# Kernel tuning notes

Hardware: AMD Instinct MI355X
Metric: run time of the kernel (lower is better)

## Reference

```python
import jax, jax.numpy as jnp
import numpy as np

NEG_SLOPE = 0.01  # nn.LeakyReLU default


def preprocess_adj(A):
    # D^-1/2 A D^-1/2, expressed as row/col broadcast scaling (same math as
    # the original diag_embed + two matmuls, without the O(N^3) waste)
    d = jnp.sum(A, axis=-1)
    d_inv_sqrt = d ** -0.5
    d_inv_sqrt = jnp.where(jnp.isinf(d_inv_sqrt), 0.0, d_inv_sqrt)
    return d_inv_sqrt[..., :, None] * A * d_inv_sqrt[..., None, :]


def gcn_layer(X, A_norm, W, b, residual=False):
    H = jax.nn.leaky_relu(jnp.einsum('bnd,df->bnf', X, W) + b, NEG_SLOPE)
    out = jnp.einsum('bnm,bmf->bnf', A_norm, H)
    if residual:
        out = out + X
    return out


def setup_inputs() -> dict:
    key = jax.random.key(0)
    ks = jax.random.split(key, 8)
    B, N, D_IN, D_H, D_OUT = 8, 2048, 128, 128, 128
    scale_in = 1.0 / np.sqrt(D_IN)
    scale_h = 1.0 / np.sqrt(D_H)
    return {
        'X': jax.random.normal(ks[0], (B, N, D_IN), dtype=jnp.float32),
        'adj': jax.random.uniform(ks[1], (B, N, N), dtype=jnp.float32),
        'W1': jax.random.uniform(ks[2], (D_IN, D_H), minval=-scale_in, maxval=scale_in),
        'b1': jax.random.uniform(ks[3], (D_H,), minval=-scale_in, maxval=scale_in),
        'W2': jax.random.uniform(ks[4], (D_H, D_H), minval=-scale_h, maxval=scale_h),
        'b2': jax.random.uniform(ks[5], (D_H,), minval=-scale_h, maxval=scale_h),
        'W3': jax.random.uniform(ks[6], (D_H, D_OUT), minval=-scale_h, maxval=scale_h),
        'b3': jax.random.uniform(ks[7], (D_OUT,), minval=-scale_h, maxval=scale_h),
    }


def reference(X, adj, W1, b1, W2, b2, W3, b3):
    # Original recomputes preprocess_adj in every layer; result is identical,
    # we honor the math (compute once since adj is unchanged across layers).
    A_norm = preprocess_adj(adj)
    X = gcn_layer(X, A_norm, W1, b1, residual=False)   # GCNLayer (norm defaults False)
    X = gcn_layer(X, A_norm, W2, b2, residual=True)    # Residual_GCNLayer
    X = gcn_layer(X, A_norm, W3, b3, residual=False)   # GCNLayer
    return X
```

## Files before the change

### kernel.cpp

```cpp
#include <hip/hip_runtime.h>


typedef short bf16x8 __attribute__((ext_vector_type(8)));
typedef float f32x4 __attribute__((ext_vector_type(4)));

static __device__ __forceinline__ float bf2f(unsigned short h) {
    union { unsigned int u; float f; } v; v.u = ((unsigned int)h) << 16; return v.f;
}
static __device__ __forceinline__ unsigned short f2bf(float x) {
    union { float f; unsigned int u; } v; v.f = x;
    return (unsigned short)((v.u + 0x7FFFu + ((v.u >> 16) & 1u)) >> 16);
}

__global__ __launch_bounds__(256) void k_pre(const float* __restrict__ adj,
                                             const float* __restrict__ W1,
                                             const float* __restrict__ W2,
                                             const float* __restrict__ W3,
                                             const float* __restrict__ b1,
                                             const float* __restrict__ b2,
                                             const float* __restrict__ b3,
                                             float* __restrict__ dinv,
                                             unsigned short* __restrict__ adjb,
                                             unsigned short* __restrict__ WT,
                                             float* __restrict__ biasf) {
    if (blockIdx.x >= 16384) {
        const int e = (blockIdx.x - 16384) * 256 + threadIdx.x;
        if (e < 49152) {
            const int w = e >> 14, r = e & 16383;
            const int f = r & 127, k = r >> 7;
            const float* W = (w == 0) ? W1 : ((w == 1) ? W2 : W3);
            WT[w * 16384 + f * 128 + k] = f2bf(W[r]);
        } else if (e < 49536) {
            const int idx = e - 49152;
            const float* bp = (idx < 128) ? b1 : ((idx < 256) ? b2 : b3);
            biasf[idx] = bp[idx & 127];
        }
        return;
    }
    const int row = blockIdx.x;
    const size_t base = (size_t)row * 2048 + threadIdx.x * 8;
    const float4 a = *(const float4*)(adj + base);
    const float4 b = *(const float4*)(adj + base + 4);
    float s = a.x + a.y + a.z + a.w + b.x + b.y + b.z + b.w;
    union { uint4 u; unsigned short h[8]; } pk;
    pk.h[0] = f2bf(a.x); pk.h[1] = f2bf(a.y); pk.h[2] = f2bf(a.z); pk.h[3] = f2bf(a.w);
    pk.h[4] = f2bf(b.x); pk.h[5] = f2bf(b.y); pk.h[6] = f2bf(b.z); pk.h[7] = f2bf(b.w);
    *(uint4*)(adjb + base) = pk.u;
#pragma unroll
    for (int off = 32; off > 0; off >>= 1) s += __shfl_down(s, off);
    __shared__ float ws[4];
    if ((threadIdx.x & 63) == 0) ws[threadIdx.x >> 6] = s;
    __syncthreads();
    if (threadIdx.x == 0) {
        float t = ws[0] + ws[1] + ws[2] + ws[3];
        dinv[row] = (t > 0.f) ? rsqrtf(t) : 0.f;
    }
}

template <int AEXT>
__global__ __launch_bounds__(256) void k_gxw(const void* __restrict__ Asrc,
                                             const unsigned short* __restrict__ WTb,
                                             const float* __restrict__ biasf,
                                             const float* __restrict__ dinv,
                                             unsigned short* __restrict__ HsT) {
    constexpr int LDK = 136;
    __shared__ unsigned short Bs[128 * LDK];

    const int tid  = threadIdx.x;
    const int wave = tid >> 6;
    const int lane = tid & 63;
    const int n_   = lane & 15;
    const int q    = lane >> 4;
    const int wm   = wave >> 1;
    const int ch   = wave & 1;

    const int r0 = blockIdx.x * 32;

#pragma unroll
    for (int it = 0; it < 8; ++it) {
        int task = tid + it * 256;
        int f  = task >> 4;
        int cj = (task & 15) * 8;
        *(uint4*)(&Bs[f * LDK + cj]) = *(const uint4*)(WTb + f * 128 + cj);
    }
    __syncthreads();

    const int arow = r0 + wm * 16 + n_;
    bf16x8 av[4];
#pragma unroll
    for (int s = 0; s < 4; ++s) {
        if (AEXT) {
            const float* p = (const float*)Asrc + (size_t)arow * 128 + s * 32 + q * 8;
            float4 uu = ((const float4*)p)[0], w = ((const float4*)p)[1];
            union { bf16x8 v; unsigned short h[8]; } r;
            r.h[0] = f2bf(uu.x); r.h[1] = f2bf(uu.y); r.h[2] = f2bf(uu.z); r.h[3] = f2bf(uu.w);
            r.h[4] = f2bf(w.x);  r.h[5] = f2bf(w.y);  r.h[6] = f2bf(w.z);  r.h[7] = f2bf(w.w);
            av[s] = r.v;
        } else {
            av[s] = *(const bf16x8*)((const unsigned short*)Asrc + (size_t)arow * 128 + s * 32 + q * 8);
        }
    }

    f32x4 acc[4];
#pragma unroll
    for (int i = 0; i < 4; ++i) acc[i] = (f32x4){0.f, 0.f, 0.f, 0.f};
#pragma unroll
    for (int s = 0; s < 4; ++s) {
#pragma unroll
        for (int nt = 0; nt < 4; ++nt) {
            bf16x8 bv = *(const bf16x8*)(&Bs[(ch * 64 + nt * 16 + n_) * LDK + s * 32 + q * 8]);
            acc[nt] = __builtin_amdgcn_mfma_f32_16x16x32_bf16(av[s], bv, acc[nt], 0, 0, 0);
        }
    }

    const int rbase = r0 + wm * 16 + q * 4;
    float dsc[4];
#pragma unroll
    for (int r = 0; r < 4; ++r) dsc[r] = dinv[rbase + r];
    const int b  = rbase >> 11;
    const int jb = rbase & 2047;
    unsigned short* Hb = HsT + (size_t)b * (128 * 2048);
#pragma unroll
    for (int nt = 0; nt < 4; ++nt) {
        const int f = ch * 64 + nt * 16 + n_;
        const float bf = biasf[f];
        unsigned short pk[4];
#pragma unroll
        for (int r = 0; r < 4; ++r) {
            float v = acc[nt][r] + bf;
            v = (v > 0.f) ? v : 0.01f * v;
            pk[r] = f2bf(v * dsc[r]);
        }
        uint2 uo;
        uo.x = (unsigned int)pk[0] | ((unsigned int)pk[1] << 16);
        uo.y = (unsigned int)pk[2] | ((unsigned int)pk[3] << 16);
        *(uint2*)(Hb + (size_t)f * 2048 + jb) = uo;
    }
}

template <int MODE, int OUT32>
__global__ __launch_bounds__(256) void k_gah(const unsigned short* __restrict__ adjb,
                                             const unsigned short* __restrict__ HsT,
                                             const float* __restrict__ dinv,
                                             const unsigned short* __restrict__ resid,
                                             void* __restrict__ outp) {
    constexpr int LDK = 72;
    constexpr int ASZ = 32 * LDK;
    constexpr int BSZ = 128 * LDK;
    __shared__ unsigned short Sm[2 * (ASZ + BSZ)];

    const int tid  = threadIdx.x;
    const int wave = tid >> 6;
    const int lane = tid & 63;
    const int n_   = lane & 15;
    const int q    = lane >> 4;

    const int bb = blockIdx.x;
    const int b  = bb & 7;
    const int rt = bb >> 3;
    const int row0 = b * 2048 + rt * 32;

    const unsigned short* Ag = adjb + (size_t)row0 * 2048;
    const unsigned short* Bg = HsT + (size_t)b * (128 * 2048);

    const int srow = tid >> 3;
    const int sc   = (tid & 7) * 8;
    const unsigned short* As = Ag + (size_t)srow * 2048 + sc;
    const unsigned short* Bsc = Bg + (size_t)srow * 2048 + sc;
    const int dA = srow * LDK + sc;
    const int dB = ASZ + srow * LDK + sc;

    uint4 rA, rB0, rB1, rB2, rB3;
    rA  = *(const uint4*)(As);
    rB0 = *(const uint4*)(Bsc);
    rB1 = *(const uint4*)(Bsc + 32 * 2048);
    rB2 = *(const uint4*)(Bsc + 64 * 2048);
    rB3 = *(const uint4*)(Bsc + 96 * 2048);
    *(uint4*)(&Sm[dA]) = rA;
    *(uint4*)(&Sm[dB]) = rB0;
    *(uint4*)(&Sm[dB + 32 * LDK]) = rB1;
    *(uint4*)(&Sm[dB + 64 * LDK]) = rB2;
    *(uint4*)(&Sm[dB + 96 * LDK]) = rB3;
    __syncthreads();

    f32x4 acc[2][2];
#pragma unroll
    for (int i = 0; i < 2; ++i)
#pragma unroll
        for (int j = 0; j < 2; ++j) acc[i][j] = (f32x4){0.f, 0.f, 0.f, 0.f};

    const int aoff = n_ * LDK + q * 8;
    const int boff = ASZ + (wave * 32 + n_) * LDK + q * 8;

#pragma unroll 1
    for (int kc = 0; kc < 32; ++kc) {
        const int cur = kc & 1;
        if (kc < 31) {
            const int kn = (kc + 1) * 64;
            rA  = *(const uint4*)(As + kn);
            rB0 = *(const uint4*)(Bsc + kn);
            rB1 = *(const uint4*)(Bsc + 32 * 2048 + kn);
            rB2 = *(const uint4*)(Bsc + 64 * 2048 + kn);
            rB3 = *(const uint4*)(Bsc + 96 * 2048 + kn);
        }
        const unsigned short* sb = &Sm[cur * (ASZ + BSZ)];
#pragma unroll
        for (int s = 0; s < 2; ++s) {
            bf16x8 a0 = *(const bf16x8*)(&sb[aoff + s * 32]);
            bf16x8 a1 = *(const bf16x8*)(&sb[aoff + 16 * LDK + s * 32]);
            bf16x8 b0 = *(const bf16x8*)(&sb[boff + s * 32]);
            bf16x8 b1 = *(const bf16x8*)(&sb[boff + 16 * LDK + s * 32]);
            acc[0][0] = __builtin_amdgcn_mfma_f32_16x16x32_bf16(a0, b0, acc[0][0], 0, 0, 0);
            acc[1][0] = __builtin_amdgcn_mfma_f32_16x16x32_bf16(a1, b0, acc[1][0], 0, 0, 0);
            acc[0][1] = __builtin_amdgcn_mfma_f32_16x16x32_bf16(a0, b1, acc[0][1], 0, 0, 0);
            acc[1][1] = __builtin_amdgcn_mfma_f32_16x16x32_bf16(a1, b1, acc[1][1], 0, 0, 0);
        }
        if (kc < 31) {
            unsigned short* sw = &Sm[(cur ^ 1) * (ASZ + BSZ)];
            *(uint4*)(&sw[dA]) = rA;
            *(uint4*)(&sw[dB]) = rB0;
            *(uint4*)(&sw[dB + 32 * LDK]) = rB1;
            *(uint4*)(&sw[dB + 64 * LDK]) = rB2;
            *(uint4*)(&sw[dB + 96 * LDK]) = rB3;
        }
        __syncthreads();
    }

    const int rb = row0 + q * 4;
    float dsc[2][4];
#pragma unroll
    for (int mi = 0; mi < 2; ++mi)
#pragma unroll
        for (int r = 0; r < 4; ++r) dsc[mi][r] = dinv[rb + mi * 16 + r];
#pragma unroll
    for (int mi = 0; mi < 2; ++mi) {
#pragma unroll
        for (int nj = 0; nj < 2; ++nj) {
            const int f = wave * 32 + nj * 16 + n_;
#pragma unroll
            for (int r = 0; r < 4; ++r) {
                const size_t gr = (size_t)(rb + mi * 16 + r);
                float v = acc[mi][nj][r] * dsc[mi][r];
                if (MODE == 2) v += bf2f(resid[gr * 128 + f]);
                if (OUT32) ((float*)outp)[gr * 128 + f] = v;
                else ((unsigned short*)outp)[gr * 128 + f] = f2bf(v);
            }
        }
    }
}

extern "C" void kernel_launch(void* const* d_in, const int* in_sizes, int n_in,
                              void* d_out, int out_size, void* d_ws, size_t ws_size,
                              hipStream_t stream) {
    const float* X   = (const float*)d_in[0];
    const float* adj = (const float*)d_in[1];
    const float* W1  = (const float*)d_in[2];
    const float* b1  = (const float*)d_in[3];
    const float* W2  = (const float*)d_in[4];
    const float* b2  = (const float*)d_in[5];
    const float* W3  = (const float*)d_in[6];
    const float* b3  = (const float*)d_in[7];

    char* ws = (char*)d_ws;
    unsigned short* adjb  = (unsigned short*)ws;
    float*          dinv  = (float*)(ws + (64u << 20));
    float*          biasf = (float*)(ws + (64u << 20) + (64u << 10));
    unsigned short* WT    = (unsigned short*)(ws + (64u << 20) + (128u << 10));
    unsigned short* HsT   = (unsigned short*)(ws + (64u << 20) + (256u << 10));
    unsigned short* Xa    = (unsigned short*)(ws + (68u << 20) + (256u << 10));
    unsigned short* X2    = (unsigned short*)(ws + (72u << 20) + (256u << 10));

    k_pre<<<16578, 256, 0, stream>>>(adj, W1, W2, W3, b1, b2, b3, dinv, adjb, WT, biasf);

    k_gxw<1><<<512, 256, 0, stream>>>(X, WT, biasf, dinv, HsT);
    k_gah<1, 0><<<512, 256, 0, stream>>>(adjb, HsT, dinv, nullptr, Xa);
    k_gxw<0><<<512, 256, 0, stream>>>(Xa, WT + 16384, biasf + 128, dinv, HsT);
    k_gah<2, 0><<<512, 256, 0, stream>>>(adjb, HsT, dinv, Xa, X2);
    k_gxw<0><<<512, 256, 0, stream>>>(X2, WT + 32768, biasf + 256, dinv, HsT);
    k_gah<1, 1><<<512, 256, 0, stream>>>(adjb, HsT, dinv, nullptr, (float*)d_out);
}
```

Measured before the change: 289.8 us.

## Load B operand directly from global into registers, shrink LDS to A tiles

The H^T (B) operand is no longer staged through shared memory. Each wave loads its own MFMA fragments straight from global memory into registers, prefetched two k-steps ahead, while only the adjacency A tile stays double-buffered in LDS. The loop is unrolled by two with a deeper prefetch distance. This cuts LDS traffic and shared memory size, which may allow higher occupancy. In exchange, each B element is read from global by every wave that needs it, with less coalesced 16-byte accesses per lane, and register pressure rises.

```diff
diff --git a/kernel.cpp b/kernel.cpp
--- a/kernel.cpp
+++ b/kernel.cpp
@@ -146,8 +146,7 @@
                                              void* __restrict__ outp) {
     constexpr int LDK = 72;
     constexpr int ASZ = 32 * LDK;
-    constexpr int BSZ = 128 * LDK;
-    __shared__ unsigned short Sm[2 * (ASZ + BSZ)];
+    __shared__ unsigned short Sm[2 * ASZ];
 
     const int tid  = threadIdx.x;
     const int wave = tid >> 6;
@@ -166,64 +165,87 @@
     const int srow = tid >> 3;
     const int sc   = (tid & 7) * 8;
     const unsigned short* As = Ag + (size_t)srow * 2048 + sc;
-    const unsigned short* Bsc = Bg + (size_t)srow * 2048 + sc;
     const int dA = srow * LDK + sc;
-    const int dB = ASZ + srow * LDK + sc;
-
-    uint4 rA, rB0, rB1, rB2, rB3;
-    rA  = *(const uint4*)(As);
-    rB0 = *(const uint4*)(Bsc);
-    rB1 = *(const uint4*)(Bsc + 32 * 2048);
-    rB2 = *(const uint4*)(Bsc + 64 * 2048);
-    rB3 = *(const uint4*)(Bsc + 96 * 2048);
-    *(uint4*)(&Sm[dA]) = rA;
-    *(uint4*)(&Sm[dB]) = rB0;
-    *(uint4*)(&Sm[dB + 32 * LDK]) = rB1;
-    *(uint4*)(&Sm[dB + 64 * LDK]) = rB2;
-    *(uint4*)(&Sm[dB + 96 * LDK]) = rB3;
+
+    const unsigned short* Bp0 = Bg + (size_t)(wave * 32 + n_) * 2048 + q * 8;
+    const unsigned short* Bp1 = Bp0 + 16 * 2048;
+
+    f32x4 acc[2][2];
+#pragma unroll
+    for (int i = 0; i < 2; ++i)
+#pragma unroll
+        for (int j = 0; j < 2; ++j) acc[i][j] = (f32x4){0.f, 0.f, 0.f, 0.f};
+
+    {
+        uint4 t0 = *(const uint4*)(As);
+        *(uint4*)(&Sm[dA]) = t0;
+    }
+    uint4 rA0 = *(const uint4*)(As + 64);
+    uint4 rA1 = *(const uint4*)(As + 128);
+    bf16x8 p00 = *(const bf16x8*)(Bp0);
+    bf16x8 p01 = *(const bf16x8*)(Bp0 + 32);
+    bf16x8 p02 = *(const bf16x8*)(Bp1);
+    bf16x8 p03 = *(const bf16x8*)(Bp1 + 32);
+    bf16x8 r00 = *(const bf16x8*)(Bp0 + 64);
+    bf16x8 r01 = *(const bf16x8*)(Bp0 + 96);
+    bf16x8 r02 = *(const bf16x8*)(Bp1 + 64);
+    bf16x8 r03 = *(const bf16x8*)(Bp1 + 96);
     __syncthreads();
 
-    f32x4 acc[2][2];
-#pragma unroll
-    for (int i = 0; i < 2; ++i)
-#pragma unroll
-        for (int j = 0; j < 2; ++j) acc[i][j] = (f32x4){0.f, 0.f, 0.f, 0.f};
-
     const int aoff = n_ * LDK + q * 8;
-    const int boff = ASZ + (wave * 32 + n_) * LDK + q * 8;
 
 #pragma unroll 1
-    for (int kc = 0; kc < 32; ++kc) {
-        const int cur = kc & 1;
-        if (kc < 31) {
-            const int kn = (kc + 1) * 64;
-            rA  = *(const uint4*)(As + kn);
-            rB0 = *(const uint4*)(Bsc + kn);
-            rB1 = *(const uint4*)(Bsc + 32 * 2048 + kn);
-            rB2 = *(const uint4*)(Bsc + 64 * 2048 + kn);
-            rB3 = *(const uint4*)(Bsc + 96 * 2048 + kn);
-        }
-        const unsigned short* sb = &Sm[cur * (ASZ + BSZ)];
-#pragma unroll
-        for (int s = 0; s < 2; ++s) {
-            bf16x8 a0 = *(const bf16x8*)(&sb[aoff + s * 32]);
-            bf16x8 a1 = *(const bf16x8*)(&sb[aoff + 16 * LDK + s * 32]);
-            bf16x8 b0 = *(const bf16x8*)(&sb[boff + s * 32]);
-            bf16x8 b1 = *(const bf16x8*)(&sb[boff + 16 * LDK + s * 32]);
-            acc[0][0] = __builtin_amdgcn_mfma_f32_16x16x32_bf16(a0, b0, acc[0][0], 0, 0, 0);
-            acc[1][0] = __builtin_amdgcn_mfma_f32_16x16x32_bf16(a1, b0, acc[1][0], 0, 0, 0);
-            acc[0][1] = __builtin_amdgcn_mfma_f32_16x16x32_bf16(a0, b1, acc[0][1], 0, 0, 0);
-            acc[1][1] = __builtin_amdgcn_mfma_f32_16x16x32_bf16(a1, b1, acc[1][1], 0, 0, 0);
-        }
-        if (kc < 31) {
-            unsigned short* sw = &Sm[(cur ^ 1) * (ASZ + BSZ)];
-            *(uint4*)(&sw[dA]) = rA;
-            *(uint4*)(&sw[dB]) = rB0;
-            *(uint4*)(&sw[dB + 32 * LDK]) = rB1;
-            *(uint4*)(&sw[dB + 64 * LDK]) = rB2;
-            *(uint4*)(&sw[dB + 96 * LDK]) = rB3;
-        }
-        __syncthreads();
+    for (int kc = 0; kc < 32; kc += 2) {
+        {
+            *(uint4*)(&Sm[ASZ + dA]) = rA0;
+            if (kc < 29) rA0 = *(const uint4*)(As + (kc + 3) * 64);
+            const unsigned short* sb = &Sm[0];
+            bf16x8 a00 = *(const bf16x8*)(&sb[aoff]);
+            bf16x8 a10 = *(const bf16x8*)(&sb[aoff + 16 * LDK]);
+            bf16x8 a01 = *(const bf16x8*)(&sb[aoff + 32]);
+            bf16x8 a11 = *(const bf16x8*)(&sb[aoff + 16 * LDK + 32]);
+            acc[0][0] = __builtin_amdgcn_mfma_f32_16x16x32_bf16(a00, p00, acc[0][0], 0, 0, 0);
+            acc[1][0] = __builtin_amdgcn_mfma_f32_16x16x32_bf16(a10, p00, acc[1][0], 0, 0, 0);
+            acc[0][1] = __builtin_amdgcn_mfma_f32_16x16x32_bf16(a00, p02, acc[0][1], 0, 0, 0);
+            acc[1][1] = __builtin_amdgcn_mfma_f32_16x16x32_bf16(a10, p02, acc[1][1], 0, 0, 0);
+            acc[0][0] = __builtin_amdgcn_mfma_f32_16x16x32_bf16(a01, p01, acc[0][0], 0, 0, 0);
+            acc[1][0] = __builtin_amdgcn_mfma_f32_16x16x32_bf16(a11, p01, acc[1][0], 0, 0, 0);
+            acc[0][1] = __builtin_amdgcn_mfma_f32_16x16x32_bf16(a01, p03, acc[0][1], 0, 0, 0);
+            acc[1][1] = __builtin_amdgcn_mfma_f32_16x16x32_bf16(a11, p03, acc[1][1], 0, 0, 0);
+            if (kc < 30) {
+                p00 = *(const bf16x8*)(Bp0 + (kc + 2) * 64);
+                p01 = *(const bf16x8*)(Bp0 + (kc + 2) * 64 + 32);
+                p02 = *(const bf16x8*)(Bp1 + (kc + 2) * 64);
+                p03 = *(const bf16x8*)(Bp1 + (kc + 2) * 64 + 32);
+            }
+            __syncthreads();
+        }
+        {
+            if (kc < 30) {
+                *(uint4*)(&Sm[dA]) = rA1;
+                if (kc < 28) rA1 = *(const uint4*)(As + (kc + 4) * 64);
+            }
+            const unsigned short* sb = &Sm[ASZ];
+            bf16x8 a00 = *(const bf16x8*)(&sb[aoff]);
+            bf16x8 a10 = *(const bf16x8*)(&sb[aoff + 16 * LDK]);
+            bf16x8 a01 = *(const bf16x8*)(&sb[aoff + 32]);
+            bf16x8 a11 = *(const bf16x8*)(&sb[aoff + 16 * LDK + 32]);
+            acc[0][0] = __builtin_amdgcn_mfma_f32_16x16x32_bf16(a00, r00, acc[0][0], 0, 0, 0);
+            acc[1][0] = __builtin_amdgcn_mfma_f32_16x16x32_bf16(a10, r00, acc[1][0], 0, 0, 0);
+            acc[0][1] = __builtin_amdgcn_mfma_f32_16x16x32_bf16(a00, r02, acc[0][1], 0, 0, 0);
+            acc[1][1] = __builtin_amdgcn_mfma_f32_16x16x32_bf16(a10, r02, acc[1][1], 0, 0, 0);
+            acc[0][0] = __builtin_amdgcn_mfma_f32_16x16x32_bf16(a01, r01, acc[0][0], 0, 0, 0);
+            acc[1][0] = __builtin_amdgcn_mfma_f32_16x16x32_bf16(a11, r01, acc[1][0], 0, 0, 0);
+            acc[0][1] = __builtin_amdgcn_mfma_f32_16x16x32_bf16(a01, r03, acc[0][1], 0, 0, 0);
+            acc[1][1] = __builtin_amdgcn_mfma_f32_16x16x32_bf16(a11, r03, acc[1][1], 0, 0, 0);
+            if (kc < 29) {
+                r00 = *(const bf16x8*)(Bp0 + (kc + 3) * 64);
+                r01 = *(const bf16x8*)(Bp0 + (kc + 3) * 64 + 32);
+                r02 = *(const bf16x8*)(Bp1 + (kc + 3) * 64);
+                r03 = *(const bf16x8*)(Bp1 + (kc + 3) * 64 + 32);
+            }
+            __syncthreads();
+        }
     }
 
     const int rb = row0 + q * 4;
```

Result: slower. 326.8 us (+12.8%).

## Use direct global-to-LDS loads with triple buffering and XOR swizzle in aggregation

Applied to the files above, without the earlier changes.

Replaces register-staged global loads plus LDS stores in the A·H aggregation kernel with global_load_lds DMA into a three-stage LDS ring. The layout switches from padded rows to an XOR-swizzled unpadded layout to avoid bank conflicts. Waits use a manual vmcnt and raw barriers, and launch bounds now request two blocks per CU. This is meant to cut VGPR pressure and instruction overhead and to deepen load overlap. It relies on precise waitcnt accounting, and the wrap-around prefetch at the end of the loop issues redundant loads.

```diff
diff --git a/kernel.cpp b/kernel.cpp
--- a/kernel.cpp
+++ b/kernel.cpp
@@ -10,6 +10,13 @@
 static __device__ __forceinline__ unsigned short f2bf(float x) {
     union { float f; unsigned int u; } v; v.f = x;
     return (unsigned short)((v.u + 0x7FFFu + ((v.u >> 16) & 1u)) >> 16);
+}
+
+static __device__ __forceinline__ void gl2lds16(const unsigned short* g,
+                                                unsigned short* l) {
+    __builtin_amdgcn_global_load_lds(
+        (const __attribute__((address_space(1))) unsigned int*)g,
+        (__attribute__((address_space(3))) unsigned int*)l, 16, 0, 0);
 }
 
 __global__ __launch_bounds__(256) void k_pre(const float* __restrict__ adj,
@@ -139,15 +146,13 @@
 }
 
 template <int MODE, int OUT32>
-__global__ __launch_bounds__(256) void k_gah(const unsigned short* __restrict__ adjb,
-                                             const unsigned short* __restrict__ HsT,
-                                             const float* __restrict__ dinv,
-                                             const unsigned short* __restrict__ resid,
-                                             void* __restrict__ outp) {
-    constexpr int LDK = 72;
-    constexpr int ASZ = 32 * LDK;
-    constexpr int BSZ = 128 * LDK;
-    __shared__ unsigned short Sm[2 * (ASZ + BSZ)];
+__global__ __launch_bounds__(256, 2) void k_gah(const unsigned short* __restrict__ adjb,
+                                                const unsigned short* __restrict__ HsT,
+                                                const float* __restrict__ dinv,
+                                                const unsigned short* __restrict__ resid,
+                                                void* __restrict__ outp) {
+    constexpr int BUFE = 10240;
+    __shared__ unsigned short Sm[3 * BUFE];
 
     const int tid  = threadIdx.x;
     const int wave = tid >> 6;
@@ -163,25 +168,28 @@
     const unsigned short* Ag = adjb + (size_t)row0 * 2048;
     const unsigned short* Bg = HsT + (size_t)b * (128 * 2048);
 
-    const int srow = tid >> 3;
-    const int sc   = (tid & 7) * 8;
-    const unsigned short* As = Ag + (size_t)srow * 2048 + sc;
-    const unsigned short* Bsc = Bg + (size_t)srow * 2048 + sc;
-    const int dA = srow * LDK + sc;
-    const int dB = ASZ + srow * LDK + sc;
-
-    uint4 rA, rB0, rB1, rB2, rB3;
-    rA  = *(const uint4*)(As);
-    rB0 = *(const uint4*)(Bsc);
-    rB1 = *(const uint4*)(Bsc + 32 * 2048);
-    rB2 = *(const uint4*)(Bsc + 64 * 2048);
-    rB3 = *(const uint4*)(Bsc + 96 * 2048);
-    *(uint4*)(&Sm[dA]) = rA;
-    *(uint4*)(&Sm[dB]) = rB0;
-    *(uint4*)(&Sm[dB + 32 * LDK]) = rB1;
-    *(uint4*)(&Sm[dB + 64 * LDK]) = rB2;
-    *(uint4*)(&Sm[dB + 96 * LDK]) = rB3;
-    __syncthreads();
+    const int lr  = lane >> 3;
+    const int sch = (lane & 7) ^ lr;
+    const unsigned short* Asg = Ag + (size_t)(wave * 8 + lr) * 2048 + sch * 8;
+    const unsigned short* Bsg0 = Bg + (size_t)(wave * 32 + 0 + lr) * 2048 + sch * 8;
+    const unsigned short* Bsg1 = Bsg0 + 8 * 2048;
+    const unsigned short* Bsg2 = Bsg0 + 16 * 2048;
+    const unsigned short* Bsg3 = Bsg0 + 24 * 2048;
+    const int dstA = wave * 512;
+    const int dstB = 2048 + wave * 2048;
+
+    const int swz = n_ & 7;
+    int aoff[2][2], boff[2][2];
+#pragma unroll
+    for (int mi = 0; mi < 2; ++mi)
+#pragma unroll
+        for (int s = 0; s < 2; ++s)
+            aoff[mi][s] = (n_ + mi * 16) * 64 + (((s * 4 + q) ^ swz) * 8);
+#pragma unroll
+    for (int nj = 0; nj < 2; ++nj)
+#pragma unroll
+        for (int s = 0; s < 2; ++s)
+            boff[nj][s] = 2048 + (wave * 32 + nj * 16 + n_) * 64 + (((s * 4 + q) ^ swz) * 8);
 
     f32x4 acc[2][2];
 #pragma unroll
@@ -189,41 +197,48 @@
 #pragma unroll
         for (int j = 0; j < 2; ++j) acc[i][j] = (f32x4){0.f, 0.f, 0.f, 0.f};
 
-    const int aoff = n_ * LDK + q * 8;
-    const int boff = ASZ + (wave * 32 + n_) * LDK + q * 8;
-
+#pragma unroll
+    for (int t = 0; t < 3; ++t) {
+        const int kofs = t * 64;
+        unsigned short* base = &Sm[t * BUFE];
+        gl2lds16(Asg + kofs, base + dstA);
+        gl2lds16(Bsg0 + kofs, base + dstB);
+        gl2lds16(Bsg1 + kofs, base + dstB + 512);
+        gl2lds16(Bsg2 + kofs, base + dstB + 1024);
+        gl2lds16(Bsg3 + kofs, base + dstB + 1536);
+    }
+
+    int cur = 0;
 #pragma unroll 1
-    for (int kc = 0; kc < 32; ++kc) {
-        const int cur = kc & 1;
-        if (kc < 31) {
-            const int kn = (kc + 1) * 64;
-            rA  = *(const uint4*)(As + kn);
-            rB0 = *(const uint4*)(Bsc + kn);
-            rB1 = *(const uint4*)(Bsc + 32 * 2048 + kn);
-            rB2 = *(const uint4*)(Bsc + 64 * 2048 + kn);
-            rB3 = *(const uint4*)(Bsc + 96 * 2048 + kn);
-        }
-        const unsigned short* sb = &Sm[cur * (ASZ + BSZ)];
+    for (int t = 0; t < 32; ++t) {
+        asm volatile("s_waitcnt vmcnt(10)" ::: "memory");
+        __builtin_amdgcn_s_barrier();
+        asm volatile("" ::: "memory");
+        const unsigned short* sb = &Sm[cur * BUFE];
 #pragma unroll
         for (int s = 0; s < 2; ++s) {
-            bf16x8 a0 = *(const bf16x8*)(&sb[aoff + s * 32]);
-            bf16x8 a1 = *(const bf16x8*)(&sb[aoff + 16 * LDK + s * 32]);
-            bf16x8 b0 = *(const bf16x8*)(&sb[boff + s * 32]);
-            bf16x8 b1 = *(const bf16x8*)(&sb[boff + 16 * LDK + s * 32]);
+            bf16x8 a0 = *(const bf16x8*)(sb + aoff[0][s]);
+            bf16x8 a1 = *(const bf16x8*)(sb + aoff[1][s]);
+            bf16x8 b0 = *(const bf16x8*)(sb + boff[0][s]);
+            bf16x8 b1 = *(const bf16x8*)(sb + boff[1][s]);
             acc[0][0] = __builtin_amdgcn_mfma_f32_16x16x32_bf16(a0, b0, acc[0][0], 0, 0, 0);
             acc[1][0] = __builtin_amdgcn_mfma_f32_16x16x32_bf16(a1, b0, acc[1][0], 0, 0, 0);
             acc[0][1] = __builtin_amdgcn_mfma_f32_16x16x32_bf16(a0, b1, acc[0][1], 0, 0, 0);
             acc[1][1] = __builtin_amdgcn_mfma_f32_16x16x32_bf16(a1, b1, acc[1][1], 0, 0, 0);
         }
-        if (kc < 31) {
-            unsigned short* sw = &Sm[(cur ^ 1) * (ASZ + BSZ)];
-            *(uint4*)(&sw[dA]) = rA;
-            *(uint4*)(&sw[dB]) = rB0;
-            *(uint4*)(&sw[dB + 32 * LDK]) = rB1;
-            *(uint4*)(&sw[dB + 64 * LDK]) = rB2;
-            *(uint4*)(&sw[dB + 96 * LDK]) = rB3;
-        }
-        __syncthreads();
+        asm volatile("" ::: "memory");
+        __builtin_amdgcn_s_barrier();
+        asm volatile("" ::: "memory");
+        {
+            const int kofs = ((t + 3) & 31) * 64;
+            unsigned short* base = &Sm[cur * BUFE];
+            gl2lds16(Asg + kofs, base + dstA);
+            gl2lds16(Bsg0 + kofs, base + dstB);
+            gl2lds16(Bsg1 + kofs, base + dstB + 512);
+            gl2lds16(Bsg2 + kofs, base + dstB + 1024);
+            gl2lds16(Bsg3 + kofs, base + dstB + 1536);
+        }
+        cur = (cur == 2) ? 0 : cur + 1;
     }
 
     const int rb = row0 + q * 4;
```

Measured after the change: 277.7 us. -4.2%, faster.
